# Performance work log

Measured on AMD Instinct MI355X. Metric: run time of the kernel, lower is better.

Reference implementation:

```python
import jax, jax.numpy as jnp
import numpy as np

N, E, D, H, O = 10000, 640000, 128, 256, 1


def setup_inputs() -> dict:
    key = jax.random.key(0)
    ks = jax.random.split(key, 10)
    s = 0.05
    return {
        "x": jax.random.normal(ks[0], (N, D), dtype=jnp.float32),
        "edge_index": jax.random.randint(ks[1], (2, E), 0, N, dtype=jnp.int64),
        # GraphConv (PyG): lin_rel (with bias) applied to sum-aggregated neighbors,
        # lin_root (no bias) applied to self features.
        "W_rel": jax.random.normal(ks[2], (D, D), dtype=jnp.float32) * s,
        "b_rel": jnp.zeros((D,), dtype=jnp.float32),
        "W_root": jax.random.normal(ks[3], (D, D), dtype=jnp.float32) * s,
        # MLP: D -> H -> H -> O, ReLU between layers
        "W1": jax.random.normal(ks[4], (H, D), dtype=jnp.float32) * s,
        "b1": jnp.zeros((H,), dtype=jnp.float32),
        "W2": jax.random.normal(ks[5], (H, H), dtype=jnp.float32) * s,
        "b2": jnp.zeros((H,), dtype=jnp.float32),
        "W3": jax.random.normal(ks[6], (O, H), dtype=jnp.float32) * s,
        "b3": jnp.zeros((O,), dtype=jnp.float32),
    }


def reference(x, edge_index, W_rel, b_rel, W_root, W1, b1, W2, b2, W3, b3):
    src, dst = edge_index[0], edge_index[1]
    # gather source features along edges, scatter-add to destinations
    agg = jax.ops.segment_sum(x[src], dst, num_segments=N)  # [N, D]
    h = agg @ W_rel.T + b_rel + x @ W_root.T                 # GraphConv out [N, D]
    h = jax.nn.relu(h @ W1.T + b1)
    h = jax.nn.relu(h @ W2.T + b2)
    h = h @ W3.T + b3                                        # [N, O]
    return jax.nn.sigmoid(h)
```

## Files before the change

### kernel.cpp

```cpp
#include <hip/hip_runtime.h>
#include <hip/hip_bf16.h>
#include <cmath>

constexpr int N_NODES = 10000;
constexpr int D_IN = 128;
constexpr int H_DIM = 256;

constexpr int NB = 157;
constexpr int BCAP = 8192;
constexpr int EPB_A = 4096;

typedef unsigned short u16;
typedef short bf16x8 __attribute__((ext_vector_type(8)));
typedef float f32x4 __attribute__((ext_vector_type(4)));

__device__ inline u16 f2bf(float f) {
    return __builtin_bit_cast(u16, __float2bfloat16(f));
}
__device__ inline float bf2f(u16 u) {
    unsigned int v = (unsigned int)u << 16;
    return __builtin_bit_cast(float, v);
}

constexpr int PREP_XB = 1250, PREP_WB = 128;
__global__ __launch_bounds__(256)
void prep_kernel(const float* __restrict__ x,
                 const float* __restrict__ W_rel, const float* __restrict__ W_root,
                 const float* __restrict__ W1, const float* __restrict__ W2,
                 u16* __restrict__ x_bf, u16* __restrict__ A0,
                 u16* __restrict__ Wcat, u16* __restrict__ W1b, u16* __restrict__ W2b,
                 int* __restrict__ gcnt) {
    const int bid = blockIdx.x, t = threadIdx.x;
    if (bid < PREP_XB) {
        int idx = bid * 256 + t;
        if (idx >= N_NODES * 32) return;
        int row = idx >> 5, c = (idx & 31) * 4;
        float4 v = *reinterpret_cast<const float4*>(x + (size_t)row * D_IN + c);
        ushort4 o;
        o.x = f2bf(v.x); o.y = f2bf(v.y); o.z = f2bf(v.z); o.w = f2bf(v.w);
        *reinterpret_cast<ushort4*>(x_bf + (size_t)row * D_IN + c) = o;
        *reinterpret_cast<ushort4*>(A0 + (size_t)row * 256 + 128 + c) = o;
    } else if (bid < PREP_XB + PREP_WB) {
        int idx4 = ((bid - PREP_XB) * 256 + t) * 4;
        const float* src;
        u16* dst;
        if (idx4 < 32768) {
            int n = idx4 >> 8, k = idx4 & 255;
            src = (k < 128) ? W_rel + n * 128 + k : W_root + n * 128 + (k - 128);
            dst = Wcat + idx4;
        } else if (idx4 < 65536) {
            src = W1 + (idx4 - 32768);
            dst = W1b + (idx4 - 32768);
        } else {
            src = W2 + (idx4 - 65536);
            dst = W2b + (idx4 - 65536);
        }
        float4 v = *reinterpret_cast<const float4*>(src);
        ushort4 o;
        o.x = f2bf(v.x); o.y = f2bf(v.y); o.z = f2bf(v.z); o.w = f2bf(v.w);
        *reinterpret_cast<ushort4*>(dst) = o;
    } else {
        if (t < NB) gcnt[t] = 0;
    }
}

__global__ __launch_bounds__(256)
void binsort_a(const int* __restrict__ ei, int* __restrict__ gcnt,
               int* __restrict__ buckets, int E) {
    __shared__ int lcnt[NB], gbase[NB];
    const int t = threadIdx.x;
    for (int i = t; i < NB; i += 256) lcnt[i] = 0;
    __syncthreads();
    const int e0 = blockIdx.x * EPB_A + t;
    int packed[16], lpos[16], bb[16];
#pragma unroll
    for (int j = 0; j < 16; ++j) {
        int e = e0 + j * 256;
        if (e < E) {
            int s = ei[e], d = ei[E + e];
            int b = d >> 6;
            bb[j] = b;
            packed[j] = ((d & 63) << 16) | s;
            lpos[j] = atomicAdd(&lcnt[b], 1);
        } else bb[j] = -1;
    }
    __syncthreads();
    for (int i = t; i < NB; i += 256)
        gbase[i] = atomicAdd(&gcnt[i], lcnt[i]);
    __syncthreads();
#pragma unroll
    for (int j = 0; j < 16; ++j)
        if (bb[j] >= 0)
            buckets[bb[j] * BCAP + gbase[bb[j]] + lpos[j]] = packed[j];
}

__global__ __launch_bounds__(256)
void binsort_b(const int* __restrict__ gcnt, const int* __restrict__ buckets,
               int* __restrict__ sorted_src, int* __restrict__ offsets, int E) {
    __shared__ int edges[BCAP];
    __shared__ int deg[64], cur[64];
    __shared__ int sbase;
    const int b = blockIdx.x, t = threadIdx.x;
    if (t < 64) {
        int v[3], sum = 0;
#pragma unroll
        for (int j = 0; j < 3; ++j) {
            int idx = t * 3 + j;
            int d = (idx < NB) ? gcnt[idx] : 0;
            v[j] = sum;
            sum += d;
        }
        int incl = sum;
#pragma unroll
        for (int off = 1; off < 64; off <<= 1) {
            int o = __shfl_up(incl, off);
            if (t >= off) incl += o;
        }
        int excl = incl - sum;
#pragma unroll
        for (int j = 0; j < 3; ++j)
            if (t * 3 + j == b) sbase = excl + v[j];
    }
    if (t < 64) deg[t] = 0;
    if (b == 0 && t == 0) offsets[N_NODES] = E;
    __syncthreads();
    const int base = sbase;
    int cnt = gcnt[b]; if (cnt > BCAP) cnt = BCAP;
    for (int i = t; i < cnt; i += 256) {
        int p = buckets[b * BCAP + i];
        edges[i] = p;
        atomicAdd(&deg[p >> 16], 1);
    }
    __syncthreads();
    if (t < 64) {
        int d = deg[t];
        int incl = d;
#pragma unroll
        for (int off = 1; off < 64; off <<= 1) {
            int o = __shfl_up(incl, off);
            if (t >= off) incl += o;
        }
        int excl = incl - d;
        cur[t] = excl;
        int node = b * 64 + t;
        if (node < N_NODES) offsets[node] = base + excl;
    }
    __syncthreads();
    for (int i = t; i < cnt; i += 256) {
        int p = edges[i];
        int pos = atomicAdd(&cur[p >> 16], 1);
        sorted_src[base + pos] = p & 0xffff;
    }
}

__global__ __launch_bounds__(256)
void gather_sum_kernel(const u16* __restrict__ x_bf,
                       const int* __restrict__ offsets,
                       const int* __restrict__ sorted_src,
                       u16* __restrict__ A0, int M) {
    int wid = (blockIdx.x * blockDim.x + threadIdx.x) >> 6;
    if (wid >= M) return;
    int lane = threadIdx.x & 63;
    int c = (lane & 31) * 4;
    int r = lane >> 5;
    int beg = offsets[wid], end = offsets[wid + 1];
    int half = (end - beg + 1) >> 1;
    int i = r ? beg + half : beg;
    const int i1 = r ? end : beg + half;
    float4 a0 = {0, 0, 0, 0}, a1 = {0, 0, 0, 0}, a2 = {0, 0, 0, 0}, a3 = {0, 0, 0, 0};
    for (; i + 4 <= i1; i += 4) {
        int s0 = sorted_src[i + 0], s1 = sorted_src[i + 1];
        int s2 = sorted_src[i + 2], s3 = sorted_src[i + 3];
        ushort4 v0 = *reinterpret_cast<const ushort4*>(x_bf + (size_t)s0 * D_IN + c);
        ushort4 v1 = *reinterpret_cast<const ushort4*>(x_bf + (size_t)s1 * D_IN + c);
        ushort4 v2 = *reinterpret_cast<const ushort4*>(x_bf + (size_t)s2 * D_IN + c);
        ushort4 v3 = *reinterpret_cast<const ushort4*>(x_bf + (size_t)s3 * D_IN + c);
        a0.x += bf2f(v0.x); a0.y += bf2f(v0.y); a0.z += bf2f(v0.z); a0.w += bf2f(v0.w);
        a1.x += bf2f(v1.x); a1.y += bf2f(v1.y); a1.z += bf2f(v1.z); a1.w += bf2f(v1.w);
        a2.x += bf2f(v2.x); a2.y += bf2f(v2.y); a2.z += bf2f(v2.z); a2.w += bf2f(v2.w);
        a3.x += bf2f(v3.x); a3.y += bf2f(v3.y); a3.z += bf2f(v3.z); a3.w += bf2f(v3.w);
    }
    for (; i < i1; ++i) {
        int s = sorted_src[i];
        ushort4 v = *reinterpret_cast<const ushort4*>(x_bf + (size_t)s * D_IN + c);
        a0.x += bf2f(v.x); a0.y += bf2f(v.y); a0.z += bf2f(v.z); a0.w += bf2f(v.w);
    }
    a0.x += a1.x + a2.x + a3.x;
    a0.y += a1.y + a2.y + a3.y;
    a0.z += a1.z + a2.z + a3.z;
    a0.w += a1.w + a2.w + a3.w;
    a0.x += __shfl_xor(a0.x, 32);
    a0.y += __shfl_xor(a0.y, 32);
    a0.z += __shfl_xor(a0.z, 32);
    a0.w += __shfl_xor(a0.w, 32);
    if (r == 0) {
        ushort4 o;
        o.x = f2bf(a0.x); o.y = f2bf(a0.y); o.z = f2bf(a0.z); o.w = f2bf(a0.w);
        *reinterpret_cast<ushort4*>(A0 + (size_t)wid * 256 + c) = o;
    }
}

__global__ __launch_bounds__(256)
void fused_mlp(const u16* __restrict__ A0, const u16* __restrict__ Wcat,
               const u16* __restrict__ W1b, const u16* __restrict__ W2b,
               const float* __restrict__ b_rel, const float* __restrict__ b1,
               const float* __restrict__ b2, const float* __restrict__ W3,
               const float* __restrict__ b3, float* __restrict__ out, int M) {
    __shared__ u16 sm[25600];
    __shared__ float part[64][2];
    u16* bufA  = sm;
    u16* bufH0 = sm + 16896;
    const int t = threadIdx.x, b = blockIdx.x;
    const int w = t >> 6, lane = t & 63;
    const int wm = w >> 1, wn = w & 1;
    const int l16 = lane & 15, q = lane >> 4;
    const int r0 = b * 64;

    for (int idx = t; idx < 2048; idx += 256) {
        int row = idx >> 5, kc = (idx & 31) * 8;
        int gr = r0 + row; if (gr >= M) gr = M - 1;
        bf16x8 v = *reinterpret_cast<const bf16x8*>(A0 + (size_t)gr * 256 + kc);
        *reinterpret_cast<bf16x8*>(bufA + row * 264 + kc) = v;
    }
    __syncthreads();

    {
        f32x4 acc[2][4] = {};
#pragma unroll
        for (int k0 = 0; k0 < 256; k0 += 32) {
            bf16x8 af[2];
#pragma unroll
            for (int i = 0; i < 2; ++i)
                af[i] = *reinterpret_cast<const bf16x8*>(
                    bufA + (wm * 32 + i * 16 + l16) * 264 + k0 + q * 8);
#pragma unroll
            for (int jj = 0; jj < 4; ++jj) {
                int col = wn * 64 + jj * 16 + l16;
                bf16x8 bfv = *reinterpret_cast<const bf16x8*>(
                    Wcat + (size_t)col * 256 + k0 + q * 8);
                acc[0][jj] = __builtin_amdgcn_mfma_f32_16x16x32_bf16(af[0], bfv, acc[0][jj], 0, 0, 0);
                acc[1][jj] = __builtin_amdgcn_mfma_f32_16x16x32_bf16(af[1], bfv, acc[1][jj], 0, 0, 0);
            }
        }
#pragma unroll
        for (int i = 0; i < 2; ++i)
#pragma unroll
            for (int jj = 0; jj < 4; ++jj) {
                int col = wn * 64 + jj * 16 + l16;
                float bb = b_rel[col];
#pragma unroll
                for (int r = 0; r < 4; ++r) {
                    int row = wm * 32 + i * 16 + q * 4 + r;
                    bufH0[row * 136 + col] = f2bf(acc[i][jj][r] + bb);
                }
            }
    }
    __syncthreads();

    {
        f32x4 acc[2][8] = {};
#pragma unroll
        for (int k0 = 0; k0 < 128; k0 += 32) {
            bf16x8 af[2];
#pragma unroll
            for (int i = 0; i < 2; ++i)
                af[i] = *reinterpret_cast<const bf16x8*>(
                    bufH0 + (wm * 32 + i * 16 + l16) * 136 + k0 + q * 8);
#pragma unroll
            for (int jj = 0; jj < 8; ++jj) {
                int col = wn * 128 + jj * 16 + l16;
                bf16x8 bfv = *reinterpret_cast<const bf16x8*>(
                    W1b + (size_t)col * 128 + k0 + q * 8);
                acc[0][jj] = __builtin_amdgcn_mfma_f32_16x16x32_bf16(af[0], bfv, acc[0][jj], 0, 0, 0);
                acc[1][jj] = __builtin_amdgcn_mfma_f32_16x16x32_bf16(af[1], bfv, acc[1][jj], 0, 0, 0);
            }
        }
#pragma unroll
        for (int i = 0; i < 2; ++i)
#pragma unroll
            for (int jj = 0; jj < 8; ++jj) {
                int col = wn * 128 + jj * 16 + l16;
                float bb = b1[col];
#pragma unroll
                for (int r = 0; r < 4; ++r) {
                    int row = wm * 32 + i * 16 + q * 4 + r;
                    bufA[row * 264 + col] = f2bf(fmaxf(acc[i][jj][r] + bb, 0.f));
                }
            }
    }
    __syncthreads();

    {
        f32x4 acc[2][8] = {};
#pragma unroll
        for (int k0 = 0; k0 < 256; k0 += 32) {
            bf16x8 af[2];
#pragma unroll
            for (int i = 0; i < 2; ++i)
                af[i] = *reinterpret_cast<const bf16x8*>(
                    bufA + (wm * 32 + i * 16 + l16) * 264 + k0 + q * 8);
#pragma unroll
            for (int jj = 0; jj < 8; ++jj) {
                int col = wn * 128 + jj * 16 + l16;
                bf16x8 bfv = *reinterpret_cast<const bf16x8*>(
                    W2b + (size_t)col * 256 + k0 + q * 8);
                acc[0][jj] = __builtin_amdgcn_mfma_f32_16x16x32_bf16(af[0], bfv, acc[0][jj], 0, 0, 0);
                acc[1][jj] = __builtin_amdgcn_mfma_f32_16x16x32_bf16(af[1], bfv, acc[1][jj], 0, 0, 0);
            }
        }
        float s[2][4] = {};
#pragma unroll
        for (int jj = 0; jj < 8; ++jj) {
            int col = wn * 128 + jj * 16 + l16;
            float bb = b2[col], ww = W3[col];
#pragma unroll
            for (int i = 0; i < 2; ++i)
#pragma unroll
                for (int r = 0; r < 4; ++r)
                    s[i][r] = fmaf(fmaxf(acc[i][jj][r] + bb, 0.f), ww, s[i][r]);
        }
#pragma unroll
        for (int off = 1; off < 16; off <<= 1)
#pragma unroll
            for (int i = 0; i < 2; ++i)
#pragma unroll
                for (int r = 0; r < 4; ++r)
                    s[i][r] += __shfl_xor(s[i][r], off);
        if (l16 == 0)
#pragma unroll
            for (int i = 0; i < 2; ++i)
#pragma unroll
                for (int r = 0; r < 4; ++r)
                    part[wm * 32 + i * 16 + q * 4 + r][wn] = s[i][r];
    }
    __syncthreads();
    if (t < 64) {
        int node = r0 + t;
        if (node < M) {
            float v = part[t][0] + part[t][1] + b3[0];
            out[node] = 1.0f / (1.0f + expf(-v));
        }
    }
}

extern "C" void kernel_launch(void* const* d_in, const int* in_sizes, int n_in,
                              void* d_out, int out_size, void* d_ws, size_t ws_size,
                              hipStream_t stream) {
    const float* x      = (const float*)d_in[0];
    const int*   ei     = (const int*)d_in[1];
    const float* W_rel  = (const float*)d_in[2];
    const float* b_rel  = (const float*)d_in[3];
    const float* W_root = (const float*)d_in[4];
    const float* W1     = (const float*)d_in[5];
    const float* b1     = (const float*)d_in[6];
    const float* W2     = (const float*)d_in[7];
    const float* b2     = (const float*)d_in[8];
    const float* W3     = (const float*)d_in[9];
    const float* b3     = (const float*)d_in[10];
    float* out = (float*)d_out;
    const int E = in_sizes[1] / 2;

    char* p = (char*)d_ws;
    auto carve = [&](size_t bytes) { char* r = p; p += (bytes + 63) & ~size_t(63); return r; };
    u16* A0   = (u16*)carve((size_t)N_NODES * 256 * 2);
    u16* x_bf = (u16*)carve((size_t)N_NODES * D_IN * 2);
    u16* Wcat = (u16*)carve(128 * 256 * 2);
    u16* W1b  = (u16*)carve(256 * 128 * 2);
    u16* W2b  = (u16*)carve(256 * 256 * 2);
    int* offsets    = (int*)carve((N_NODES + 4) * 4);
    int* gcnt       = (int*)carve(NB * 4);
    int* buckets    = (int*)carve((size_t)NB * BCAP * 4);
    int* sorted_src = (int*)carve((size_t)E * 4);

    prep_kernel<<<PREP_XB + PREP_WB + 1, 256, 0, stream>>>(
        x, W_rel, W_root, W1, W2, x_bf, A0, Wcat, W1b, W2b, gcnt);
    binsort_a<<<(E + EPB_A - 1) / EPB_A, 256, 0, stream>>>(ei, gcnt, buckets, E);
    binsort_b<<<NB, 256, 0, stream>>>(gcnt, buckets, sorted_src, offsets, E);
    gather_sum_kernel<<<(N_NODES * 64 + 255) / 256, 256, 0, stream>>>(
        x_bf, offsets, sorted_src, A0, N_NODES);
    fused_mlp<<<(N_NODES + 63) / 64, 256, 0, stream>>>(
        A0, Wcat, W1b, W2b, b_rel, b1, b2, W3, b3, out, N_NODES);
}
```

Baseline: 152.8 us.

## Fuse bucket sort, neighbor gather and MLP into one per-bucket kernel

Merges binsort_b, gather_sum_kernel and fused_mlp into one 512-thread kernel per 64-node bucket. The CSR is now built in shared memory, aggregated rows go straight into the LDS A-tile, and the global A0, offsets and sorted_src arrays are dropped along with two launches. This removes global round-trips and launch gaps. In exchange only 157 blocks run, each doing a long serial sort-gather-GEMM chain, so parallelism and latency hiding during the gather may suffer. The larger LDS footprint also limits occupancy.

```diff
diff --git a/kernel.cpp b/kernel.cpp
--- a/kernel.cpp
+++ b/kernel.cpp
@@ -27,7 +27,7 @@
 void prep_kernel(const float* __restrict__ x,
                  const float* __restrict__ W_rel, const float* __restrict__ W_root,
                  const float* __restrict__ W1, const float* __restrict__ W2,
-                 u16* __restrict__ x_bf, u16* __restrict__ A0,
+                 u16* __restrict__ x_bf,
                  u16* __restrict__ Wcat, u16* __restrict__ W1b, u16* __restrict__ W2b,
                  int* __restrict__ gcnt) {
     const int bid = blockIdx.x, t = threadIdx.x;
@@ -39,7 +39,6 @@
         ushort4 o;
         o.x = f2bf(v.x); o.y = f2bf(v.y); o.z = f2bf(v.z); o.w = f2bf(v.w);
         *reinterpret_cast<ushort4*>(x_bf + (size_t)row * D_IN + c) = o;
-        *reinterpret_cast<ushort4*>(A0 + (size_t)row * 256 + 128 + c) = o;
     } else if (bid < PREP_XB + PREP_WB) {
         int idx4 = ((bid - PREP_XB) * 256 + t) * 4;
         const float* src;
@@ -94,159 +93,128 @@
             buckets[bb[j] * BCAP + gbase[bb[j]] + lpos[j]] = packed[j];
 }
 
-__global__ __launch_bounds__(256)
-void binsort_b(const int* __restrict__ gcnt, const int* __restrict__ buckets,
-               int* __restrict__ sorted_src, int* __restrict__ offsets, int E) {
+__global__ __launch_bounds__(512)
+void mega_kernel(const int* __restrict__ gcnt, const int* __restrict__ buckets,
+                 const u16* __restrict__ x_bf,
+                 const u16* __restrict__ Wcat, const u16* __restrict__ W1b,
+                 const u16* __restrict__ W2b,
+                 const float* __restrict__ b_rel, const float* __restrict__ b1,
+                 const float* __restrict__ b2, const float* __restrict__ W3,
+                 const float* __restrict__ b3, float* __restrict__ out, int M) {
     __shared__ int edges[BCAP];
-    __shared__ int deg[64], cur[64];
-    __shared__ int sbase;
+    __shared__ u16 ssrc[BCAP];
+    __shared__ u16 bufA[64 * 264];
+    __shared__ u16 bufH0[64 * 136];
+    __shared__ int deg[64], cur[64], sbeg[64];
+    __shared__ float part[64][4];
     const int b = blockIdx.x, t = threadIdx.x;
+    const int w = t >> 6, lane = t & 63;
+    const int wm = w >> 2, wn = w & 3;
+    const int l16 = lane & 15, q = lane >> 4;
+    const int r0 = b * 64;
+
+    if (t < 64) deg[t] = 0;
+    __syncthreads();
+    int cnt = gcnt[b]; if (cnt > BCAP) cnt = BCAP;
+    for (int i = t; i < cnt; i += 512) {
+        int p = buckets[b * BCAP + i];
+        edges[i] = p;
+        atomicAdd(&deg[p >> 16], 1);
+    }
+    __syncthreads();
     if (t < 64) {
-        int v[3], sum = 0;
-#pragma unroll
-        for (int j = 0; j < 3; ++j) {
-            int idx = t * 3 + j;
-            int d = (idx < NB) ? gcnt[idx] : 0;
-            v[j] = sum;
-            sum += d;
-        }
-        int incl = sum;
+        int d = deg[t];
+        int incl = d;
 #pragma unroll
         for (int off = 1; off < 64; off <<= 1) {
             int o = __shfl_up(incl, off);
             if (t >= off) incl += o;
         }
-        int excl = incl - sum;
-#pragma unroll
-        for (int j = 0; j < 3; ++j)
-            if (t * 3 + j == b) sbase = excl + v[j];
-    }
-    if (t < 64) deg[t] = 0;
-    if (b == 0 && t == 0) offsets[N_NODES] = E;
-    __syncthreads();
-    const int base = sbase;
-    int cnt = gcnt[b]; if (cnt > BCAP) cnt = BCAP;
-    for (int i = t; i < cnt; i += 256) {
-        int p = buckets[b * BCAP + i];
-        edges[i] = p;
-        atomicAdd(&deg[p >> 16], 1);
-    }
-    __syncthreads();
-    if (t < 64) {
-        int d = deg[t];
-        int incl = d;
-#pragma unroll
-        for (int off = 1; off < 64; off <<= 1) {
-            int o = __shfl_up(incl, off);
-            if (t >= off) incl += o;
-        }
         int excl = incl - d;
         cur[t] = excl;
-        int node = b * 64 + t;
-        if (node < N_NODES) offsets[node] = base + excl;
-    }
-    __syncthreads();
-    for (int i = t; i < cnt; i += 256) {
+        sbeg[t] = excl;
+    }
+    __syncthreads();
+    for (int i = t; i < cnt; i += 512) {
         int p = edges[i];
         int pos = atomicAdd(&cur[p >> 16], 1);
-        sorted_src[base + pos] = p & 0xffff;
-    }
-}
-
-__global__ __launch_bounds__(256)
-void gather_sum_kernel(const u16* __restrict__ x_bf,
-                       const int* __restrict__ offsets,
-                       const int* __restrict__ sorted_src,
-                       u16* __restrict__ A0, int M) {
-    int wid = (blockIdx.x * blockDim.x + threadIdx.x) >> 6;
-    if (wid >= M) return;
-    int lane = threadIdx.x & 63;
-    int c = (lane & 31) * 4;
-    int r = lane >> 5;
-    int beg = offsets[wid], end = offsets[wid + 1];
-    int half = (end - beg + 1) >> 1;
-    int i = r ? beg + half : beg;
-    const int i1 = r ? end : beg + half;
-    float4 a0 = {0, 0, 0, 0}, a1 = {0, 0, 0, 0}, a2 = {0, 0, 0, 0}, a3 = {0, 0, 0, 0};
-    for (; i + 4 <= i1; i += 4) {
-        int s0 = sorted_src[i + 0], s1 = sorted_src[i + 1];
-        int s2 = sorted_src[i + 2], s3 = sorted_src[i + 3];
-        ushort4 v0 = *reinterpret_cast<const ushort4*>(x_bf + (size_t)s0 * D_IN + c);
-        ushort4 v1 = *reinterpret_cast<const ushort4*>(x_bf + (size_t)s1 * D_IN + c);
-        ushort4 v2 = *reinterpret_cast<const ushort4*>(x_bf + (size_t)s2 * D_IN + c);
-        ushort4 v3 = *reinterpret_cast<const ushort4*>(x_bf + (size_t)s3 * D_IN + c);
-        a0.x += bf2f(v0.x); a0.y += bf2f(v0.y); a0.z += bf2f(v0.z); a0.w += bf2f(v0.w);
-        a1.x += bf2f(v1.x); a1.y += bf2f(v1.y); a1.z += bf2f(v1.z); a1.w += bf2f(v1.w);
-        a2.x += bf2f(v2.x); a2.y += bf2f(v2.y); a2.z += bf2f(v2.z); a2.w += bf2f(v2.w);
-        a3.x += bf2f(v3.x); a3.y += bf2f(v3.y); a3.z += bf2f(v3.z); a3.w += bf2f(v3.w);
-    }
-    for (; i < i1; ++i) {
-        int s = sorted_src[i];
-        ushort4 v = *reinterpret_cast<const ushort4*>(x_bf + (size_t)s * D_IN + c);
-        a0.x += bf2f(v.x); a0.y += bf2f(v.y); a0.z += bf2f(v.z); a0.w += bf2f(v.w);
-    }
-    a0.x += a1.x + a2.x + a3.x;
-    a0.y += a1.y + a2.y + a3.y;
-    a0.z += a1.z + a2.z + a3.z;
-    a0.w += a1.w + a2.w + a3.w;
-    a0.x += __shfl_xor(a0.x, 32);
-    a0.y += __shfl_xor(a0.y, 32);
-    a0.z += __shfl_xor(a0.z, 32);
-    a0.w += __shfl_xor(a0.w, 32);
-    if (r == 0) {
-        ushort4 o;
-        o.x = f2bf(a0.x); o.y = f2bf(a0.y); o.z = f2bf(a0.z); o.w = f2bf(a0.w);
-        *reinterpret_cast<ushort4*>(A0 + (size_t)wid * 256 + c) = o;
-    }
-}
-
-__global__ __launch_bounds__(256)
-void fused_mlp(const u16* __restrict__ A0, const u16* __restrict__ Wcat,
-               const u16* __restrict__ W1b, const u16* __restrict__ W2b,
-               const float* __restrict__ b_rel, const float* __restrict__ b1,
-               const float* __restrict__ b2, const float* __restrict__ W3,
-               const float* __restrict__ b3, float* __restrict__ out, int M) {
-    __shared__ u16 sm[25600];
-    __shared__ float part[64][2];
-    u16* bufA  = sm;
-    u16* bufH0 = sm + 16896;
-    const int t = threadIdx.x, b = blockIdx.x;
-    const int w = t >> 6, lane = t & 63;
-    const int wm = w >> 1, wn = w & 1;
-    const int l16 = lane & 15, q = lane >> 4;
-    const int r0 = b * 64;
-
-    for (int idx = t; idx < 2048; idx += 256) {
-        int row = idx >> 5, kc = (idx & 31) * 8;
+        ssrc[pos] = (u16)(p & 0xffff);
+    }
+    for (int idx = t; idx < 64 * 16; idx += 512) {
+        int row = idx >> 4, kc = (idx & 15) * 8;
         int gr = r0 + row; if (gr >= M) gr = M - 1;
-        bf16x8 v = *reinterpret_cast<const bf16x8*>(A0 + (size_t)gr * 256 + kc);
-        *reinterpret_cast<bf16x8*>(bufA + row * 264 + kc) = v;
-    }
-    __syncthreads();
-
+        bf16x8 v = *reinterpret_cast<const bf16x8*>(x_bf + (size_t)gr * D_IN + kc);
+        *reinterpret_cast<bf16x8*>(&bufA[row * 264 + 128 + kc]) = v;
+    }
+    __syncthreads();
     {
-        f32x4 acc[2][4] = {};
+        const int c = (lane & 31) * 4;
+        const int r = lane >> 5;
+        for (int j = 0; j < 8; ++j) {
+            int ln = w * 8 + j;
+            int beg = sbeg[ln], dg = deg[ln];
+            int half = (dg + 1) >> 1;
+            int i = beg + (r ? half : 0);
+            const int i1 = r ? beg + dg : beg + half;
+            float4 a0 = {0, 0, 0, 0}, a1 = {0, 0, 0, 0};
+            float4 a2 = {0, 0, 0, 0}, a3 = {0, 0, 0, 0};
+            for (; i + 4 <= i1; i += 4) {
+                int s0 = ssrc[i + 0], s1 = ssrc[i + 1];
+                int s2 = ssrc[i + 2], s3 = ssrc[i + 3];
+                ushort4 v0 = *reinterpret_cast<const ushort4*>(x_bf + (size_t)s0 * D_IN + c);
+                ushort4 v1 = *reinterpret_cast<const ushort4*>(x_bf + (size_t)s1 * D_IN + c);
+                ushort4 v2 = *reinterpret_cast<const ushort4*>(x_bf + (size_t)s2 * D_IN + c);
+                ushort4 v3 = *reinterpret_cast<const ushort4*>(x_bf + (size_t)s3 * D_IN + c);
+                a0.x += bf2f(v0.x); a0.y += bf2f(v0.y); a0.z += bf2f(v0.z); a0.w += bf2f(v0.w);
+                a1.x += bf2f(v1.x); a1.y += bf2f(v1.y); a1.z += bf2f(v1.z); a1.w += bf2f(v1.w);
+                a2.x += bf2f(v2.x); a2.y += bf2f(v2.y); a2.z += bf2f(v2.z); a2.w += bf2f(v2.w);
+                a3.x += bf2f(v3.x); a3.y += bf2f(v3.y); a3.z += bf2f(v3.z); a3.w += bf2f(v3.w);
+            }
+            for (; i < i1; ++i) {
+                int s = ssrc[i];
+                ushort4 v = *reinterpret_cast<const ushort4*>(x_bf + (size_t)s * D_IN + c);
+                a0.x += bf2f(v.x); a0.y += bf2f(v.y); a0.z += bf2f(v.z); a0.w += bf2f(v.w);
+            }
+            a0.x += a1.x + a2.x + a3.x;
+            a0.y += a1.y + a2.y + a3.y;
+            a0.z += a1.z + a2.z + a3.z;
+            a0.w += a1.w + a2.w + a3.w;
+            a0.x += __shfl_xor(a0.x, 32);
+            a0.y += __shfl_xor(a0.y, 32);
+            a0.z += __shfl_xor(a0.z, 32);
+            a0.w += __shfl_xor(a0.w, 32);
+            if (r == 0) {
+                ushort4 o;
+                o.x = f2bf(a0.x); o.y = f2bf(a0.y); o.z = f2bf(a0.z); o.w = f2bf(a0.w);
+                *reinterpret_cast<ushort4*>(&bufA[ln * 264 + c]) = o;
+            }
+        }
+    }
+    __syncthreads();
+
+    {
+        f32x4 acc[2][2] = {};
 #pragma unroll
         for (int k0 = 0; k0 < 256; k0 += 32) {
             bf16x8 af[2];
 #pragma unroll
             for (int i = 0; i < 2; ++i)
                 af[i] = *reinterpret_cast<const bf16x8*>(
-                    bufA + (wm * 32 + i * 16 + l16) * 264 + k0 + q * 8);
-#pragma unroll
-            for (int jj = 0; jj < 4; ++jj) {
-                int col = wn * 64 + jj * 16 + l16;
-                bf16x8 bfv = *reinterpret_cast<const bf16x8*>(
+                    &bufA[(wm * 32 + i * 16 + l16) * 264 + k0 + q * 8]);
+#pragma unroll
+            for (int jj = 0; jj < 2; ++jj) {
+                int col = wn * 32 + jj * 16 + l16;
+                bf16x8 bv = *reinterpret_cast<const bf16x8*>(
                     Wcat + (size_t)col * 256 + k0 + q * 8);
-                acc[0][jj] = __builtin_amdgcn_mfma_f32_16x16x32_bf16(af[0], bfv, acc[0][jj], 0, 0, 0);
-                acc[1][jj] = __builtin_amdgcn_mfma_f32_16x16x32_bf16(af[1], bfv, acc[1][jj], 0, 0, 0);
+                acc[0][jj] = __builtin_amdgcn_mfma_f32_16x16x32_bf16(af[0], bv, acc[0][jj], 0, 0, 0);
+                acc[1][jj] = __builtin_amdgcn_mfma_f32_16x16x32_bf16(af[1], bv, acc[1][jj], 0, 0, 0);
             }
         }
 #pragma unroll
         for (int i = 0; i < 2; ++i)
 #pragma unroll
-            for (int jj = 0; jj < 4; ++jj) {
-                int col = wn * 64 + jj * 16 + l16;
+            for (int jj = 0; jj < 2; ++jj) {
+                int col = wn * 32 + jj * 16 + l16;
                 float bb = b_rel[col];
 #pragma unroll
                 for (int r = 0; r < 4; ++r) {
@@ -258,28 +226,29 @@
     __syncthreads();
 
     {
-        f32x4 acc[2][8] = {};
+        f32x4 acc[2][4] = {};
 #pragma unroll
         for (int k0 = 0; k0 < 128; k0 += 32) {
             bf16x8 af[2];
 #pragma unroll
             for (int i = 0; i < 2; ++i)
                 af[i] = *reinterpret_cast<const bf16x8*>(
-                    bufH0 + (wm * 32 + i * 16 + l16) * 136 + k0 + q * 8);
-#pragma unroll
-            for (int jj = 0; jj < 8; ++jj) {
-                int col = wn * 128 + jj * 16 + l16;
-                bf16x8 bfv = *reinterpret_cast<const bf16x8*>(
+                    &bufH0[(wm * 32 + i * 16 + l16) * 136 + k0 + q * 8]);
+#pragma unroll
+            for (int jj = 0; jj < 4; ++jj) {
+                int col = wn * 64 + jj * 16 + l16;
+                bf16x8 bv = *reinterpret_cast<const bf16x8*>(
                     W1b + (size_t)col * 128 + k0 + q * 8);
-                acc[0][jj] = __builtin_amdgcn_mfma_f32_16x16x32_bf16(af[0], bfv, acc[0][jj], 0, 0, 0);
-                acc[1][jj] = __builtin_amdgcn_mfma_f32_16x16x32_bf16(af[1], bfv, acc[1][jj], 0, 0, 0);
-            }
-        }
+                acc[0][jj] = __builtin_amdgcn_mfma_f32_16x16x32_bf16(af[0], bv, acc[0][jj], 0, 0, 0);
+                acc[1][jj] = __builtin_amdgcn_mfma_f32_16x16x32_bf16(af[1], bv, acc[1][jj], 0, 0, 0);
+            }
+        }
+        __syncthreads();
 #pragma unroll
         for (int i = 0; i < 2; ++i)
 #pragma unroll
-            for (int jj = 0; jj < 8; ++jj) {
-                int col = wn * 128 + jj * 16 + l16;
+            for (int jj = 0; jj < 4; ++jj) {
+                int col = wn * 64 + jj * 16 + l16;
                 float bb = b1[col];
 #pragma unroll
                 for (int r = 0; r < 4; ++r) {
@@ -291,27 +260,27 @@
     __syncthreads();
 
     {
-        f32x4 acc[2][8] = {};
+        f32x4 acc[2][4] = {};
 #pragma unroll
         for (int k0 = 0; k0 < 256; k0 += 32) {
             bf16x8 af[2];
 #pragma unroll
             for (int i = 0; i < 2; ++i)
                 af[i] = *reinterpret_cast<const bf16x8*>(
-                    bufA + (wm * 32 + i * 16 + l16) * 264 + k0 + q * 8);
-#pragma unroll
-            for (int jj = 0; jj < 8; ++jj) {
-                int col = wn * 128 + jj * 16 + l16;
-                bf16x8 bfv = *reinterpret_cast<const bf16x8*>(
+                    &bufA[(wm * 32 + i * 16 + l16) * 264 + k0 + q * 8]);
+#pragma unroll
+            for (int jj = 0; jj < 4; ++jj) {
+                int col = wn * 64 + jj * 16 + l16;
+                bf16x8 bv = *reinterpret_cast<const bf16x8*>(
                     W2b + (size_t)col * 256 + k0 + q * 8);
-                acc[0][jj] = __builtin_amdgcn_mfma_f32_16x16x32_bf16(af[0], bfv, acc[0][jj], 0, 0, 0);
-                acc[1][jj] = __builtin_amdgcn_mfma_f32_16x16x32_bf16(af[1], bfv, acc[1][jj], 0, 0, 0);
+                acc[0][jj] = __builtin_amdgcn_mfma_f32_16x16x32_bf16(af[0], bv, acc[0][jj], 0, 0, 0);
+                acc[1][jj] = __builtin_amdgcn_mfma_f32_16x16x32_bf16(af[1], bv, acc[1][jj], 0, 0, 0);
             }
         }
         float s[2][4] = {};
 #pragma unroll
-        for (int jj = 0; jj < 8; ++jj) {
-            int col = wn * 128 + jj * 16 + l16;
+        for (int jj = 0; jj < 4; ++jj) {
+            int col = wn * 64 + jj * 16 + l16;
             float bb = b2[col], ww = W3[col];
 #pragma unroll
             for (int i = 0; i < 2; ++i)
@@ -337,7 +306,7 @@
     if (t < 64) {
         int node = r0 + t;
         if (node < M) {
-            float v = part[t][0] + part[t][1] + b3[0];
+            float v = part[t][0] + part[t][1] + part[t][2] + part[t][3] + b3[0];
             out[node] = 1.0f / (1.0f + expf(-v));
         }
     }
@@ -362,22 +331,16 @@
 
     char* p = (char*)d_ws;
     auto carve = [&](size_t bytes) { char* r = p; p += (bytes + 63) & ~size_t(63); return r; };
-    u16* A0   = (u16*)carve((size_t)N_NODES * 256 * 2);
     u16* x_bf = (u16*)carve((size_t)N_NODES * D_IN * 2);
     u16* Wcat = (u16*)carve(128 * 256 * 2);
     u16* W1b  = (u16*)carve(256 * 128 * 2);
     u16* W2b  = (u16*)carve(256 * 256 * 2);
-    int* offsets    = (int*)carve((N_NODES + 4) * 4);
-    int* gcnt       = (int*)carve(NB * 4);
-    int* buckets    = (int*)carve((size_t)NB * BCAP * 4);
-    int* sorted_src = (int*)carve((size_t)E * 4);
+    int* gcnt    = (int*)carve(NB * 4);
+    int* buckets = (int*)carve((size_t)NB * BCAP * 4);
 
     prep_kernel<<<PREP_XB + PREP_WB + 1, 256, 0, stream>>>(
-        x, W_rel, W_root, W1, W2, x_bf, A0, Wcat, W1b, W2b, gcnt);
+        x, W_rel, W_root, W1, W2, x_bf, Wcat, W1b, W2b, gcnt);
     binsort_a<<<(E + EPB_A - 1) / EPB_A, 256, 0, stream>>>(ei, gcnt, buckets, E);
-    binsort_b<<<NB, 256, 0, stream>>>(gcnt, buckets, sorted_src, offsets, E);
-    gather_sum_kernel<<<(N_NODES * 64 + 255) / 256, 256, 0, stream>>>(
-        x_bf, offsets, sorted_src, A0, N_NODES);
-    fused_mlp<<<(N_NODES + 63) / 64, 256, 0, stream>>>(
-        A0, Wcat, W1b, W2b, b_rel, b1, b2, W3, b3, out, N_NODES);
-}
+    mega_kernel<<<NB, 512, 0, stream>>>(gcnt, buckets, x_bf, Wcat, W1b, W2b,
+                                        b_rel, b1, b2, W3, b3, out, N_NODES);
+}
```

Result: faster. 140.5 us (-8.0%).

## Stage MLP weights in LDS and split N across eight waves

Applied to the files above, without the earlier changes.

The fused MLP kernel now uses 512 threads (8 waves, 2x4) and copies each layer's bf16 weight matrix into shared memory before its MFMA loop, rather than reading weights straight from global memory per fragment. W2 is staged in two 128-column halves, and the W3 dot-product partials are accumulated across both halves before a single reduction. This targets global/L2 traffic and latency on the B-operand loads. In exchange it adds LDS (about 120KB per block, which limits occupancy) and extra barriers for the staging copies.

```diff
diff --git a/kernel.cpp b/kernel.cpp
--- a/kernel.cpp
+++ b/kernel.cpp
@@ -200,53 +200,58 @@
     }
 }
 
-__global__ __launch_bounds__(256)
+__global__ __launch_bounds__(512)
 void fused_mlp(const u16* __restrict__ A0, const u16* __restrict__ Wcat,
                const u16* __restrict__ W1b, const u16* __restrict__ W2b,
                const float* __restrict__ b_rel, const float* __restrict__ b1,
                const float* __restrict__ b2, const float* __restrict__ W3,
                const float* __restrict__ b3, float* __restrict__ out, int M) {
-    __shared__ u16 sm[25600];
-    __shared__ float part[64][2];
-    u16* bufA  = sm;
-    u16* bufH0 = sm + 16896;
+    __shared__ u16 bufA[64 * 264];
+    __shared__ u16 bufH0[64 * 136];
+    __shared__ u16 wbuf[34816];
+    __shared__ float part[64][4];
     const int t = threadIdx.x, b = blockIdx.x;
     const int w = t >> 6, lane = t & 63;
-    const int wm = w >> 1, wn = w & 1;
+    const int wm = w >> 2, wn = w & 3;
     const int l16 = lane & 15, q = lane >> 4;
     const int r0 = b * 64;
 
-    for (int idx = t; idx < 2048; idx += 256) {
+    for (int idx = t; idx < 64 * 32; idx += 512) {
         int row = idx >> 5, kc = (idx & 31) * 8;
         int gr = r0 + row; if (gr >= M) gr = M - 1;
         bf16x8 v = *reinterpret_cast<const bf16x8*>(A0 + (size_t)gr * 256 + kc);
-        *reinterpret_cast<bf16x8*>(bufA + row * 264 + kc) = v;
+        *reinterpret_cast<bf16x8*>(&bufA[row * 264 + kc]) = v;
+    }
+    for (int idx = t; idx < 128 * 32; idx += 512) {
+        int row = idx >> 5, kc = (idx & 31) * 8;
+        bf16x8 v = *reinterpret_cast<const bf16x8*>(Wcat + (size_t)row * 256 + kc);
+        *reinterpret_cast<bf16x8*>(&wbuf[row * 264 + kc]) = v;
     }
     __syncthreads();
 
     {
-        f32x4 acc[2][4] = {};
+        f32x4 acc[2][2] = {};
 #pragma unroll
         for (int k0 = 0; k0 < 256; k0 += 32) {
             bf16x8 af[2];
 #pragma unroll
             for (int i = 0; i < 2; ++i)
                 af[i] = *reinterpret_cast<const bf16x8*>(
-                    bufA + (wm * 32 + i * 16 + l16) * 264 + k0 + q * 8);
-#pragma unroll
-            for (int jj = 0; jj < 4; ++jj) {
-                int col = wn * 64 + jj * 16 + l16;
-                bf16x8 bfv = *reinterpret_cast<const bf16x8*>(
-                    Wcat + (size_t)col * 256 + k0 + q * 8);
-                acc[0][jj] = __builtin_amdgcn_mfma_f32_16x16x32_bf16(af[0], bfv, acc[0][jj], 0, 0, 0);
-                acc[1][jj] = __builtin_amdgcn_mfma_f32_16x16x32_bf16(af[1], bfv, acc[1][jj], 0, 0, 0);
+                    &bufA[(wm * 32 + i * 16 + l16) * 264 + k0 + q * 8]);
+#pragma unroll
+            for (int jj = 0; jj < 2; ++jj) {
+                int col = wn * 32 + jj * 16 + l16;
+                bf16x8 bv = *reinterpret_cast<const bf16x8*>(
+                    &wbuf[col * 264 + k0 + q * 8]);
+                acc[0][jj] = __builtin_amdgcn_mfma_f32_16x16x32_bf16(af[0], bv, acc[0][jj], 0, 0, 0);
+                acc[1][jj] = __builtin_amdgcn_mfma_f32_16x16x32_bf16(af[1], bv, acc[1][jj], 0, 0, 0);
             }
         }
 #pragma unroll
         for (int i = 0; i < 2; ++i)
 #pragma unroll
-            for (int jj = 0; jj < 4; ++jj) {
-                int col = wn * 64 + jj * 16 + l16;
+            for (int jj = 0; jj < 2; ++jj) {
+                int col = wn * 32 + jj * 16 + l16;
                 float bb = b_rel[col];
 #pragma unroll
                 for (int r = 0; r < 4; ++r) {
@@ -257,29 +262,36 @@
     }
     __syncthreads();
 
+    for (int idx = t; idx < 256 * 16; idx += 512) {
+        int row = idx >> 4, kc = (idx & 15) * 8;
+        bf16x8 v = *reinterpret_cast<const bf16x8*>(W1b + (size_t)row * 128 + kc);
+        *reinterpret_cast<bf16x8*>(&wbuf[row * 136 + kc]) = v;
+    }
+    __syncthreads();
+
     {
-        f32x4 acc[2][8] = {};
+        f32x4 acc[2][4] = {};
 #pragma unroll
         for (int k0 = 0; k0 < 128; k0 += 32) {
             bf16x8 af[2];
 #pragma unroll
             for (int i = 0; i < 2; ++i)
                 af[i] = *reinterpret_cast<const bf16x8*>(
-                    bufH0 + (wm * 32 + i * 16 + l16) * 136 + k0 + q * 8);
-#pragma unroll
-            for (int jj = 0; jj < 8; ++jj) {
-                int col = wn * 128 + jj * 16 + l16;
-                bf16x8 bfv = *reinterpret_cast<const bf16x8*>(
-                    W1b + (size_t)col * 128 + k0 + q * 8);
-                acc[0][jj] = __builtin_amdgcn_mfma_f32_16x16x32_bf16(af[0], bfv, acc[0][jj], 0, 0, 0);
-                acc[1][jj] = __builtin_amdgcn_mfma_f32_16x16x32_bf16(af[1], bfv, acc[1][jj], 0, 0, 0);
+                    &bufH0[(wm * 32 + i * 16 + l16) * 136 + k0 + q * 8]);
+#pragma unroll
+            for (int jj = 0; jj < 4; ++jj) {
+                int col = wn * 64 + jj * 16 + l16;
+                bf16x8 bv = *reinterpret_cast<const bf16x8*>(
+                    &wbuf[col * 136 + k0 + q * 8]);
+                acc[0][jj] = __builtin_amdgcn_mfma_f32_16x16x32_bf16(af[0], bv, acc[0][jj], 0, 0, 0);
+                acc[1][jj] = __builtin_amdgcn_mfma_f32_16x16x32_bf16(af[1], bv, acc[1][jj], 0, 0, 0);
             }
         }
 #pragma unroll
         for (int i = 0; i < 2; ++i)
 #pragma unroll
-            for (int jj = 0; jj < 8; ++jj) {
-                int col = wn * 128 + jj * 16 + l16;
+            for (int jj = 0; jj < 4; ++jj) {
+                int col = wn * 64 + jj * 16 + l16;
                 float bb = b1[col];
 #pragma unroll
                 for (int r = 0; r < 4; ++r) {
@@ -288,30 +300,38 @@
                 }
             }
     }
-    __syncthreads();
-
-    {
-        f32x4 acc[2][8] = {};
+
+    float s[2][4] = {};
+#pragma unroll
+    for (int h = 0; h < 2; ++h) {
+        __syncthreads();
+        for (int idx = t; idx < 128 * 32; idx += 512) {
+            int row = idx >> 5, kc = (idx & 31) * 8;
+            bf16x8 v = *reinterpret_cast<const bf16x8*>(
+                W2b + (size_t)(h * 128 + row) * 256 + kc);
+            *reinterpret_cast<bf16x8*>(&wbuf[row * 264 + kc]) = v;
+        }
+        __syncthreads();
+        f32x4 acc[2][2] = {};
 #pragma unroll
         for (int k0 = 0; k0 < 256; k0 += 32) {
             bf16x8 af[2];
 #pragma unroll
             for (int i = 0; i < 2; ++i)
                 af[i] = *reinterpret_cast<const bf16x8*>(
-                    bufA + (wm * 32 + i * 16 + l16) * 264 + k0 + q * 8);
-#pragma unroll
-            for (int jj = 0; jj < 8; ++jj) {
-                int col = wn * 128 + jj * 16 + l16;
-                bf16x8 bfv = *reinterpret_cast<const bf16x8*>(
-                    W2b + (size_t)col * 256 + k0 + q * 8);
-                acc[0][jj] = __builtin_amdgcn_mfma_f32_16x16x32_bf16(af[0], bfv, acc[0][jj], 0, 0, 0);
-                acc[1][jj] = __builtin_amdgcn_mfma_f32_16x16x32_bf16(af[1], bfv, acc[1][jj], 0, 0, 0);
+                    &bufA[(wm * 32 + i * 16 + l16) * 264 + k0 + q * 8]);
+#pragma unroll
+            for (int jj = 0; jj < 2; ++jj) {
+                int lcol = wn * 32 + jj * 16 + l16;
+                bf16x8 bv = *reinterpret_cast<const bf16x8*>(
+                    &wbuf[lcol * 264 + k0 + q * 8]);
+                acc[0][jj] = __builtin_amdgcn_mfma_f32_16x16x32_bf16(af[0], bv, acc[0][jj], 0, 0, 0);
+                acc[1][jj] = __builtin_amdgcn_mfma_f32_16x16x32_bf16(af[1], bv, acc[1][jj], 0, 0, 0);
             }
         }
-        float s[2][4] = {};
-#pragma unroll
-        for (int jj = 0; jj < 8; ++jj) {
-            int col = wn * 128 + jj * 16 + l16;
+#pragma unroll
+        for (int jj = 0; jj < 2; ++jj) {
+            int col = h * 128 + wn * 32 + jj * 16 + l16;
             float bb = b2[col], ww = W3[col];
 #pragma unroll
             for (int i = 0; i < 2; ++i)
@@ -319,25 +339,25 @@
                 for (int r = 0; r < 4; ++r)
                     s[i][r] = fmaf(fmaxf(acc[i][jj][r] + bb, 0.f), ww, s[i][r]);
         }
-#pragma unroll
-        for (int off = 1; off < 16; off <<= 1)
-#pragma unroll
-            for (int i = 0; i < 2; ++i)
-#pragma unroll
-                for (int r = 0; r < 4; ++r)
-                    s[i][r] += __shfl_xor(s[i][r], off);
-        if (l16 == 0)
-#pragma unroll
-            for (int i = 0; i < 2; ++i)
-#pragma unroll
-                for (int r = 0; r < 4; ++r)
-                    part[wm * 32 + i * 16 + q * 4 + r][wn] = s[i][r];
-    }
+    }
+#pragma unroll
+    for (int off = 1; off < 16; off <<= 1)
+#pragma unroll
+        for (int i = 0; i < 2; ++i)
+#pragma unroll
+            for (int r = 0; r < 4; ++r)
+                s[i][r] += __shfl_xor(s[i][r], off);
+    if (l16 == 0)
+#pragma unroll
+        for (int i = 0; i < 2; ++i)
+#pragma unroll
+            for (int r = 0; r < 4; ++r)
+                part[wm * 32 + i * 16 + q * 4 + r][wn] = s[i][r];
     __syncthreads();
     if (t < 64) {
         int node = r0 + t;
         if (node < M) {
-            float v = part[t][0] + part[t][1] + b3[0];
+            float v = part[t][0] + part[t][1] + part[t][2] + part[t][3] + b3[0];
             out[node] = 1.0f / (1.0f + expf(-v));
         }
     }
@@ -378,6 +398,6 @@
     binsort_b<<<NB, 256, 0, stream>>>(gcnt, buckets, sorted_src, offsets, E);
     gather_sum_kernel<<<(N_NODES * 64 + 255) / 256, 256, 0, stream>>>(
         x_bf, offsets, sorted_src, A0, N_NODES);
-    fused_mlp<<<(N_NODES + 63) / 64, 256, 0, stream>>>(
-        A0, Wcat, W1b, W2b, b_rel, b1, b2, W3, b3, out, N_NODES);
-}
+    fused_mlp<<<NB, 512, 0, stream>>>(A0, Wcat, W1b, W2b,
+                                      b_rel, b1, b2, W3, b3, out, N_NODES);
+}
```

New measurement: 132.5 us. 1.15x faster.
